# Kernel optimization log

Measured on AMD Instinct MI355X. Metric: run time of the kernel, lower is better.

Reference implementation:

```python
import jax, jax.numpy as jnp
import numpy as np

B, S, D, H, M = 2, 2048, 1024, 16, 40
DH = D // H  # 64
L = S + M    # kv length after memory concat


def setup_inputs() -> dict:
    key = jax.random.key(0)
    ks = jax.random.split(key, 20)
    s = 1.0 / np.sqrt(D)
    inp = {
        'v': jax.random.normal(ks[0], (B, S, D), jnp.float32),
        'k': jax.random.normal(ks[1], (B, S, D), jnp.float32),
        'q': jax.random.normal(ks[2], (B, S, D), jnp.float32),
        # additive binary mask (1 = masked out), broadcast over heads
        'mask': jax.random.randint(ks[3], (B, 1, S, L), 0, 2).astype(jnp.float32),
        'Wq': jax.random.normal(ks[4], (D, D), jnp.float32) * s,
        'bq': jnp.zeros((D,), jnp.float32),
        'Wk': jax.random.normal(ks[5], (D, D), jnp.float32) * s,
        'bk': jnp.zeros((D,), jnp.float32),
        'Wv': jax.random.normal(ks[6], (D, D), jnp.float32) * s,
        'bv': jnp.zeros((D,), jnp.float32),
        'k_memory': jax.random.normal(ks[7], (1, M, D), jnp.float32) * (1.0 / np.sqrt(DH)),
        'v_memory': jax.random.normal(ks[8], (1, M, D), jnp.float32) * (1.0 / np.sqrt(M)),
        'Wkm': jax.random.normal(ks[9], (D, D), jnp.float32) * s,
        'bkm': jnp.zeros((D,), jnp.float32),
        'Wvm': jax.random.normal(ks[10], (D, D), jnp.float32) * s,
        'bvm': jnp.zeros((D,), jnp.float32),
        'Wo': jax.random.normal(ks[11], (D, D), jnp.float32) * s,
        'bo': jnp.zeros((D,), jnp.float32),
    }
    return inp


def _split_heads(x):
    # [B, T, D] -> [B, H, T, DH]
    b, t, _ = x.shape
    return x.reshape(b, t, H, DH).transpose(0, 2, 1, 3)


def reference(v, k, q, mask, Wq, bq, Wk, bk, Wv, bv, k_memory, v_memory,
              Wkm, bkm, Wvm, bvm, Wo, bo):
    qp = q @ Wq + bq
    kp = k @ Wk + bk
    vp = v @ Wv + bv
    km = (k_memory @ Wkm + bkm)  # [1, M, D]
    vm = (v_memory @ Wvm + bvm)  # [1, M, D]
    kc = jnp.concatenate([kp, jnp.broadcast_to(km, (kp.shape[0], M, D))], axis=1)
    vc = jnp.concatenate([vp, jnp.broadcast_to(vm, (vp.shape[0], M, D))], axis=1)
    qh, kh, vh = _split_heads(qp), _split_heads(kc), _split_heads(vc)
    # scores: [B, H, S, L]
    scores = jnp.einsum('bhqd,bhkd->bhqk', qh, kh) / np.sqrt(DH)
    scores = scores + mask * (-1e9)
    attn = jax.nn.softmax(scores, axis=-1)
    ctx = jnp.einsum('bhqk,bhkd->bhqd', attn, vh)  # [B, H, S, DH]
    ctx = ctx.transpose(0, 2, 1, 3).reshape(ctx.shape[0], S, D)
    out = ctx @ Wo + bo
    return (out, attn)
```

## Files before the change

### kernel.cpp

```cpp
#include <hip/hip_runtime.h>
#include <hip/hip_bf16.h>

typedef __attribute__((ext_vector_type(8))) short short8v;
typedef __attribute__((ext_vector_type(4))) short short4v;
typedef __attribute__((ext_vector_type(4))) float f32x4;

constexpr int B_ = 2, S_ = 2048, H_ = 16, MM_ = 40;
constexpr int L_ = S_ + MM_;
constexpr int LP_ = 2112;
constexpr int NT_ = 33;
constexpr float QSCALE = 0.18033688011112042f;

struct S2 { short hi, lo; };
__device__ __forceinline__ S2 split2(float f) {
    unsigned u = __builtin_bit_cast(unsigned, f);
    short hi = (short)(u >> 16);
    float fh = __builtin_bit_cast(float, u & 0xFFFF0000u);
    float fl = f - fh;
    short lo = (short)(__builtin_bit_cast(unsigned, fl) >> 16);
    return {hi, lo};
}
__device__ __forceinline__ short f2bh(float f) {
    unsigned u = __builtin_bit_cast(unsigned, f);
    u = (u + 0x7FFFu + ((u >> 16) & 1u)) >> 16;
    return (short)u;
}
__device__ __forceinline__ f32x4 mfma16(short8v a, short8v b, f32x4 c) {
    return __builtin_amdgcn_mfma_f32_16x16x32_bf16(a, b, c, 0, 0, 0);
}
__device__ __forceinline__ unsigned cvt_pk_bf16(float a, float b) {
    unsigned r;
    asm("v_cvt_pk_bf16_f32 %0, %1, %2" : "=v"(r) : "v"(a), "v"(b));
    return r;
}

__global__ __launch_bounds__(256) void wsplit6_kernel(
    const float* __restrict__ W0, const float* __restrict__ W1,
    const float* __restrict__ W2, const float* __restrict__ W3,
    const float* __restrict__ W4, const float* __restrict__ W5,
    short* __restrict__ WT)
{
    const float* Ws[6] = {W0, W1, W2, W3, W4, W5};
    const float* W = Ws[blockIdx.z];
    short* WTh = WT + (size_t)blockIdx.z * 2097152;
    short* WTl = WTh + 1048576;
    __shared__ float T[64][68];
    const int t = threadIdx.x;
    const int k0 = blockIdx.x * 64, n0 = blockIdx.y * 64;
    {
        int r = t >> 2, c = (t & 3) * 16;
        const float* src = W + (size_t)(k0 + r) * 1024 + n0 + c;
        *(float4*)&T[r][c + 0]  = *(const float4*)(src + 0);
        *(float4*)&T[r][c + 4]  = *(const float4*)(src + 4);
        *(float4*)&T[r][c + 8]  = *(const float4*)(src + 8);
        *(float4*)&T[r][c + 12] = *(const float4*)(src + 12);
    }
    __syncthreads();
    {
        int n = t >> 2, ks = (t & 3) * 16;
        short8v h0, h1, l0, l1;
#pragma unroll
        for (int j = 0; j < 8; ++j) {
            S2 a = split2(T[ks + j][n]);     h0[j] = a.hi; l0[j] = a.lo;
            S2 b = split2(T[ks + 8 + j][n]); h1[j] = b.hi; l1[j] = b.lo;
        }
        size_t dst = (size_t)(n0 + n) * 1024 + k0 + ks;
        *(short8v*)(WTh + dst) = h0;  *(short8v*)(WTh + dst + 8) = h1;
        *(short8v*)(WTl + dst) = l0;  *(short8v*)(WTl + dst + 8) = l1;
    }
}

template<int ASRC>
__device__ __forceinline__ void gemm_core(
    const float* __restrict__ Af, const short* __restrict__ Ahg,
    const short* __restrict__ Alg, const short* __restrict__ WTh,
    const short* __restrict__ WTl, const float* __restrict__ bias,
    float bscale, float scale,
    short* __restrict__ Oh, short* __restrict__ Ol, float* __restrict__ Of,
    int M, int RPB, int TD, int loff, int omode, int bx, int by,
    int kbeg, int kend)
{
    __shared__ short Ah[128][40];
    __shared__ short Al[128][40];
    __shared__ short Bh[128][40];
    __shared__ short Bl[128][40];
    const int tid = threadIdx.x;
    const int lane = tid & 63, wid = tid >> 6;
    const int wr = wid >> 1, wc = wid & 1;
    const int row0 = by * 128, col0 = bx * 128;
    const int sr = tid >> 1, sc = (tid & 1) << 4;

    f32x4 acc[4][4] = {};

    for (int k0 = kbeg; k0 < kend; k0 += 32) {
        if (ASRC == 0) {
            float f[16];
            int gr = row0 + sr;
            if (gr < M) {
                const float* ap = Af + (size_t)gr * 1024 + k0 + sc;
                float4 a0 = *(const float4*)(ap + 0);
                float4 a1 = *(const float4*)(ap + 4);
                float4 a2 = *(const float4*)(ap + 8);
                float4 a3 = *(const float4*)(ap + 12);
                f[0]=a0.x; f[1]=a0.y; f[2]=a0.z; f[3]=a0.w;
                f[4]=a1.x; f[5]=a1.y; f[6]=a1.z; f[7]=a1.w;
                f[8]=a2.x; f[9]=a2.y; f[10]=a2.z; f[11]=a2.w;
                f[12]=a3.x; f[13]=a3.y; f[14]=a3.z; f[15]=a3.w;
            } else {
#pragma unroll
                for (int j = 0; j < 16; ++j) f[j] = 0.f;
            }
            short8v h0, h1, l0, l1;
#pragma unroll
            for (int j = 0; j < 8; ++j) {
                S2 s = split2(f[j]); h0[j] = s.hi; l0[j] = s.lo;
            }
#pragma unroll
            for (int j = 0; j < 8; ++j) {
                S2 s = split2(f[8 + j]); h1[j] = s.hi; l1[j] = s.lo;
            }
            *(short8v*)&Ah[sr][sc] = h0; *(short8v*)&Ah[sr][sc + 8] = h1;
            *(short8v*)&Al[sr][sc] = l0; *(short8v*)&Al[sr][sc + 8] = l1;
        } else {
            const short* ah = Ahg + (size_t)(row0 + sr) * 1024 + k0 + sc;
            const short* al = Alg + (size_t)(row0 + sr) * 1024 + k0 + sc;
            *(short8v*)&Ah[sr][sc]     = *(const short8v*)ah;
            *(short8v*)&Ah[sr][sc + 8] = *(const short8v*)(ah + 8);
            *(short8v*)&Al[sr][sc]     = *(const short8v*)al;
            *(short8v*)&Al[sr][sc + 8] = *(const short8v*)(al + 8);
        }
        {
            const short* bh = WTh + (size_t)(col0 + sr) * 1024 + k0 + sc;
            const short* bl = WTl + (size_t)(col0 + sr) * 1024 + k0 + sc;
            *(short8v*)&Bh[sr][sc]     = *(const short8v*)bh;
            *(short8v*)&Bh[sr][sc + 8] = *(const short8v*)(bh + 8);
            *(short8v*)&Bl[sr][sc]     = *(const short8v*)bl;
            *(short8v*)&Bl[sr][sc + 8] = *(const short8v*)(bl + 8);
        }
        __syncthreads();
        const int kof = (lane >> 4) << 3;
        const int ar = lane & 15;
        short8v afh[4], afl[4], bfh[4], bfl[4];
#pragma unroll
        for (int i = 0; i < 4; ++i) {
            afh[i] = *(const short8v*)&Ah[wr * 64 + i * 16 + ar][kof];
            afl[i] = *(const short8v*)&Al[wr * 64 + i * 16 + ar][kof];
            bfh[i] = *(const short8v*)&Bh[wc * 64 + i * 16 + ar][kof];
            bfl[i] = *(const short8v*)&Bl[wc * 64 + i * 16 + ar][kof];
        }
#pragma unroll
        for (int i = 0; i < 4; ++i)
#pragma unroll
            for (int j = 0; j < 4; ++j) {
                acc[i][j] = mfma16(afh[i], bfh[j], acc[i][j]);
                acc[i][j] = mfma16(afh[i], bfl[j], acc[i][j]);
                acc[i][j] = mfma16(afl[i], bfh[j], acc[i][j]);
            }
        __syncthreads();
    }

#pragma unroll
    for (int i = 0; i < 4; ++i) {
#pragma unroll
        for (int j = 0; j < 4; ++j) {
            int colb = col0 + wc * 64 + j * 16 + (lane & 15);
            float bv = bias[colb] * bscale;
            int rowb = row0 + wr * 64 + i * 16 + ((lane >> 4) << 2);
            if (omode == 2) {
                if (rowb < M) {
                    int bb = rowb / RPB, tt = rowb % RPB;
                    int hh = colb >> 6, dh = colb & 63;
                    short4v hs;
#pragma unroll
                    for (int r = 0; r < 4; ++r)
                        hs[r] = f2bh((acc[i][j][r] + bv) * scale);
                    size_t dst = ((size_t)(bb * H_ + hh) * 64 + dh) * LP_ + loff + tt;
                    *(short4v*)(Oh + dst) = hs;
                }
            } else {
#pragma unroll
                for (int r = 0; r < 4; ++r) {
                    int row = rowb + r;
                    if (row < M) {
                        float o = (acc[i][j][r] + bv) * scale;
                        int bb = row / RPB, tt = row % RPB;
                        if (omode == 0) {
                            Of[((size_t)bb * TD + loff + tt) * 1024 + colb] = o;
                        } else {
                            int hh = colb >> 6, dh = colb & 63;
                            size_t dst = ((size_t)(bb * H_ + hh) * TD + loff + tt) * 64 + dh;
                            S2 s = split2(o);
                            Oh[dst] = s.hi; Ol[dst] = s.lo;
                        }
                    }
                }
            }
        }
    }
}

__global__ __launch_bounds__(256) void qkv_gemm(
    const float* __restrict__ q_in, const float* __restrict__ k_in,
    const float* __restrict__ v_in, const float* __restrict__ kmem,
    const float* __restrict__ vmem, const short* __restrict__ WT,
    const float* __restrict__ bq, const float* __restrict__ bk,
    const float* __restrict__ bv, const float* __restrict__ bkm,
    const float* __restrict__ bvm,
    short* __restrict__ Qh, short* __restrict__ Ql,
    short* __restrict__ Kh, short* __restrict__ Kl, short* __restrict__ Vh,
    const float* __restrict__ mask, unsigned* __restrict__ mp)
{
    const int z = blockIdx.z;
    if (z == 3) {
        const int blk = blockIdx.y * 8 + blockIdx.x;
        for (int rr = 0; rr < 16; ++rr) {
            const int row = blk * 16 + rr;
            const float* mr = mask + (size_t)row * L_;
            unsigned* orow = mp + (size_t)row * 68;
            for (int wd = threadIdx.x; wd < 66; wd += 256) {
                int l0 = wd * 32;
                unsigned bits = 0u;
                int lim = (wd < 65) ? 32 : 8;
                for (int j = 0; j < lim; j += 4) {
                    float4 m4 = *(const float4*)(mr + l0 + j);
                    bits |= ((unsigned)(m4.x != 0.f)) << (j + 0);
                    bits |= ((unsigned)(m4.y != 0.f)) << (j + 1);
                    bits |= ((unsigned)(m4.z != 0.f)) << (j + 2);
                    bits |= ((unsigned)(m4.w != 0.f)) << (j + 3);
                }
                if (wd == 65) bits |= 0xFFFFFF00u;
                orow[wd] = bits;
            }
        }
        for (int k = threadIdx.x; k < 192; k += 256) {
            int g = blk * 192 + k;
            int rd = g / 24, l = L_ + g % 24;
            Vh[(size_t)rd * LP_ + l] = 0;
        }
        return;
    }
    if (z >= 4) {
        if (blockIdx.y != 0) return;
        const int which = (z - 4) >> 1, b = (z - 4) & 1;
        const float* A = which ? vmem : kmem;
        const short* WTh = WT + (size_t)(3 + which) * 2097152;
        const short* WTl = WTh + 1048576;
        const float* bias = which ? bvm : bkm;
        short* Oh = which ? (Vh + (size_t)b * H_ * 64 * LP_)
                          : (Kh + (size_t)b * H_ * LP_ * 64);
        short* Ol = which ? nullptr : (Kl + (size_t)b * H_ * LP_ * 64);
        gemm_core<0>(A, nullptr, nullptr, WTh, WTl, bias, 1.0f, 1.0f,
                     Oh, Ol, nullptr, 40, 40, LP_, S_, which ? 2 : 1,
                     blockIdx.x, 0, 0, 1024);
        return;
    }
    const float* A = (z == 0) ? q_in : (z == 1) ? k_in : v_in;
    const short* WTh = WT + (size_t)z * 2097152;
    const short* WTl = WTh + 1048576;
    const float* bias = (z == 0) ? bq : (z == 1) ? bk : bv;
    float scale = (z == 0) ? QSCALE : 1.0f;
    short* Oh = (z == 0) ? Qh : (z == 1) ? Kh : Vh;
    short* Ol = (z == 0) ? Ql : Kl;
    int omode = (z == 2) ? 2 : 1;
    int TD = (z == 0) ? S_ : LP_;
    gemm_core<0>(A, nullptr, nullptr, WTh, WTl, bias, 1.0f, scale,
                 Oh, Ol, nullptr, 4096, 2048, TD, 0, omode,
                 blockIdx.x, blockIdx.y, 0, 1024);
}

__global__ __launch_bounds__(256) void out_gemm(
    const short* __restrict__ Ch, const short* __restrict__ Cl,
    const short* __restrict__ WT, const float* __restrict__ bo,
    float* __restrict__ Po0, float* __restrict__ Po1)
{
    const int z = blockIdx.z;
    const short* WTh = WT + (size_t)5 * 2097152;
    gemm_core<1>(nullptr, Ch, Cl, WTh, WTh + 1048576, bo,
                 z == 0 ? 1.0f : 0.0f, 1.0f,
                 nullptr, nullptr, z == 0 ? Po0 : Po1, 4096, 2048, S_, 0, 0,
                 blockIdx.x, blockIdx.y, z * 512, z * 512 + 512);
}

__global__ __launch_bounds__(256) void attn4_kernel(
    const short* __restrict__ Qh, const short* __restrict__ Ql,
    const short* __restrict__ Kh, const short* __restrict__ Kl,
    const short* __restrict__ Vh, const unsigned* __restrict__ mp,
    float* __restrict__ attn, float* __restrict__ invg,
    short* __restrict__ Ch, short* __restrict__ Cl)
{
    __shared__ short KhB[2][64][64];
    __shared__ short KlB[2][64][64];
    __shared__ short VB[64][64];
    __shared__ short Ph[4][16][68];

    const int id = blockIdx.x;
    const int wg = (id & 7) * 64 + (id >> 3);
    const int bh = wg >> 4, qb2 = wg & 15;
    const int b = bh >> 4, h = bh & 15;
    const int lane = threadIdx.x & 63, w = threadIdx.x >> 6;
    const int lq = lane & 15, hi = lane >> 4;
    const int sw = lq & 7;
    const int q0A = qb2 * 128 + w * 16;
    const int q0B = q0A + 64;

    const char* kh_g = (const char*)(Kh + (size_t)bh * LP_ * 64);
    const char* kl_g = (const char*)(Kl + (size_t)bh * LP_ * 64);
    const char* v_g  = (const char*)(Vh + (size_t)bh * 64 * LP_);

    auto stage_k = [&](int buf, int tt) {
#pragma unroll
        for (int i = 0; i < 2; ++i) {
            int o = w * 2048 + i * 1024 + lane * 16;
            int r = o >> 7, c = (o >> 4) & 7;
            int cs = c ^ (r & 7);
            const char* sh = kh_g + (size_t)tt * 8192 + r * 128 + cs * 16;
            const char* sl = kl_g + (size_t)tt * 8192 + r * 128 + cs * 16;
            __builtin_amdgcn_global_load_lds((const void*)sh,
                (void*)((char*)&KhB[buf][0][0] + w * 2048 + i * 1024), 16, 0, 0);
            __builtin_amdgcn_global_load_lds((const void*)sl,
                (void*)((char*)&KlB[buf][0][0] + w * 2048 + i * 1024), 16, 0, 0);
        }
    };
    auto stage_v = [&](int tt) {
#pragma unroll
        for (int i = 0; i < 2; ++i) {
            int o = w * 2048 + i * 1024 + lane * 16;
            int dh = o >> 7, c = (o >> 4) & 7;
            int cs = c ^ (dh & 7);
            const char* src = v_g + (size_t)dh * (LP_ * 2) + (size_t)tt * 128 + cs * 16;
            __builtin_amdgcn_global_load_lds((const void*)src,
                (void*)((char*)&VB[0][0] + w * 2048 + i * 1024), 16, 0, 0);
        }
    };

    const size_t qbA = ((size_t)bh * S_ + q0A + lq) * 64 + hi * 8;
    const size_t qbB = ((size_t)bh * S_ + q0B + lq) * 64 + hi * 8;
    const short8v qh0A = *(const short8v*)(Qh + qbA);
    const short8v qh1A = *(const short8v*)(Qh + qbA + 32);
    const short8v ql0A = *(const short8v*)(Ql + qbA);
    const short8v ql1A = *(const short8v*)(Ql + qbA + 32);
    const short8v qh0B = *(const short8v*)(Qh + qbB);
    const short8v qh1B = *(const short8v*)(Qh + qbB + 32);
    const short8v ql0B = *(const short8v*)(Ql + qbB);
    const short8v ql1B = *(const short8v*)(Ql + qbB + 32);
    const unsigned* mrowA = mp + ((size_t)b * S_ + q0A + lq) * 68;
    const unsigned* mrowB = mp + ((size_t)b * S_ + q0B + lq) * 68;

    const int dr = lane >> 2, dc = lane & 3;
    short* dbaseA = (short*)(attn + ((size_t)bh * S_ + q0A - (w * 16) + (w * 16) + dr) * L_);
    dbaseA = (short*)(attn + ((size_t)bh * S_ + q0A + dr) * L_);
    short* dbaseB = (short*)(attn + ((size_t)bh * S_ + q0B + dr) * L_);

    float smA = 0.f, smB = 0.f;
    f32x4 pvA[4] = {};
    f32x4 pvB[4] = {};

    stage_k(0, 0);
    stage_v(0);
    __syncthreads();

    int cur = 0;
    for (int t = 0; t < NT_; ++t) {
        if (t < NT_ - 1) stage_k(cur ^ 1, t + 1);

        const short8v* kp = (const short8v*)&KhB[cur][0][0];
        const short8v* lp = (const short8v*)&KlB[cur][0][0];
        short8v kh0s[4], kh1s[4], kl0s[4], kl1s[4];
#pragma unroll
        for (int ls = 0; ls < 4; ++ls) {
            const int r = ls * 16 + lq;
            kh0s[ls] = kp[r * 8 + (hi ^ sw)];
            kh1s[ls] = kp[r * 8 + ((hi + 4) ^ sw)];
            kl0s[ls] = lp[r * 8 + (hi ^ sw)];
            kl1s[ls] = lp[r * 8 + ((hi + 4) ^ sw)];
        }
        const unsigned w0A = mrowA[2 * t], w1A = mrowA[2 * t + 1];
#pragma unroll
        for (int ls = 0; ls < 4; ++ls) {
            __builtin_amdgcn_s_setprio(1);
            f32x4 acc = {0.f, 0.f, 0.f, 0.f};
            acc = mfma16(kh0s[ls], qh0A, acc); acc = mfma16(kh1s[ls], qh1A, acc);
            acc = mfma16(kh0s[ls], ql0A, acc); acc = mfma16(kh1s[ls], ql1A, acc);
            acc = mfma16(kl0s[ls], qh0A, acc); acc = mfma16(kl1s[ls], qh1A, acc);
            __builtin_amdgcn_s_setprio(0);
            const unsigned wb = (ls & 2) ? w1A : w0A;
            const int sh = (ls & 1) * 16 + hi * 4;
            float pr[4];
#pragma unroll
            for (int r2 = 0; r2 < 4; ++r2) {
                float e = __builtin_exp2f(acc[r2]);
                pr[r2] = ((wb >> (sh + r2)) & 1u) ? 0.f : e;
            }
            smA += (pr[0] + pr[1]) + (pr[2] + pr[3]);
            *(uint2*)&Ph[w][lq][ls * 16 + hi * 4] =
                uint2{cvt_pk_bf16(pr[0], pr[1]), cvt_pk_bf16(pr[2], pr[3])};
        }
        {
            short8v v0 = *(const short8v*)&Ph[w][dr][dc * 8];
            short8v v1 = *(const short8v*)&Ph[w][dr][32 + dc * 8];
            short* dst = dbaseA + t * 64 + dc * 8;
            if (t < NT_ - 1) { *(short8v*)dst = v0; *(short8v*)(dst + 32) = v1; }
            else { *(short8v*)dst = v0; if (dc == 0) *(short8v*)(dst + 32) = v1; }
        }
        __syncthreads();
        {
            const short8v pa0 = *(const short8v*)&Ph[w][lq][hi * 8];
            const short8v pa1 = *(const short8v*)&Ph[w][lq][32 + hi * 8];
            const short8v* vp = (const short8v*)&VB[0][0];
            __builtin_amdgcn_s_setprio(1);
#pragma unroll
            for (int j = 0; j < 4; ++j)
                pvA[j] = mfma16(pa0, vp[(j * 16 + lq) * 8 + (hi ^ sw)], pvA[j]);
#pragma unroll
            for (int j = 0; j < 4; ++j)
                pvA[j] = mfma16(pa1, vp[(j * 16 + lq) * 8 + ((hi + 4) ^ sw)], pvA[j]);
            __builtin_amdgcn_s_setprio(0);
        }
        const unsigned w0B = mrowB[2 * t], w1B = mrowB[2 * t + 1];
#pragma unroll
        for (int ls = 0; ls < 4; ++ls) {
            __builtin_amdgcn_s_setprio(1);
            f32x4 acc = {0.f, 0.f, 0.f, 0.f};
            acc = mfma16(kh0s[ls], qh0B, acc); acc = mfma16(kh1s[ls], qh1B, acc);
            acc = mfma16(kh0s[ls], ql0B, acc); acc = mfma16(kh1s[ls], ql1B, acc);
            acc = mfma16(kl0s[ls], qh0B, acc); acc = mfma16(kl1s[ls], qh1B, acc);
            __builtin_amdgcn_s_setprio(0);
            const unsigned wb = (ls & 2) ? w1B : w0B;
            const int sh = (ls & 1) * 16 + hi * 4;
            float pr[4];
#pragma unroll
            for (int r2 = 0; r2 < 4; ++r2) {
                float e = __builtin_exp2f(acc[r2]);
                pr[r2] = ((wb >> (sh + r2)) & 1u) ? 0.f : e;
            }
            smB += (pr[0] + pr[1]) + (pr[2] + pr[3]);
            *(uint2*)&Ph[w][lq][ls * 16 + hi * 4] =
                uint2{cvt_pk_bf16(pr[0], pr[1]), cvt_pk_bf16(pr[2], pr[3])};
        }
        {
            short8v v0 = *(const short8v*)&Ph[w][dr][dc * 8];
            short8v v1 = *(const short8v*)&Ph[w][dr][32 + dc * 8];
            short* dst = dbaseB + t * 64 + dc * 8;
            if (t < NT_ - 1) { *(short8v*)dst = v0; *(short8v*)(dst + 32) = v1; }
            else { *(short8v*)dst = v0; if (dc == 0) *(short8v*)(dst + 32) = v1; }
        }
        {
            const short8v pa0 = *(const short8v*)&Ph[w][lq][hi * 8];
            const short8v pa1 = *(const short8v*)&Ph[w][lq][32 + hi * 8];
            const short8v* vp = (const short8v*)&VB[0][0];
            __builtin_amdgcn_s_setprio(1);
#pragma unroll
            for (int j = 0; j < 4; ++j)
                pvB[j] = mfma16(pa0, vp[(j * 16 + lq) * 8 + (hi ^ sw)], pvB[j]);
#pragma unroll
            for (int j = 0; j < 4; ++j)
                pvB[j] = mfma16(pa1, vp[(j * 16 + lq) * 8 + ((hi + 4) ^ sw)], pvB[j]);
            __builtin_amdgcn_s_setprio(0);
        }
        __syncthreads();
        if (t < NT_ - 1) stage_v(t + 1);
        cur ^= 1;
    }

    smA += __shfl_xor(smA, 16); smA += __shfl_xor(smA, 32);
    smB += __shfl_xor(smB, 16); smB += __shfl_xor(smB, 32);
    if (lane < 16) {
        invg[(size_t)bh * S_ + q0A + lane] = smA > 0.f ? 1.0f / smA : 0.f;
        invg[(size_t)bh * S_ + q0B + lane] = smB > 0.f ? 1.0f / smB : 0.f;
    }
#pragma unroll
    for (int r = 0; r < 4; ++r) {
        float svA = __shfl(smA, hi * 4 + r);
        float svB = __shfl(smB, hi * 4 + r);
        float ivA = svA > 0.f ? 1.0f / svA : 0.f;
        float ivB = svB > 0.f ? 1.0f / svB : 0.f;
#pragma unroll
        for (int j = 0; j < 4; ++j) {
            size_t dA = ((size_t)b * S_ + q0A + hi * 4 + r) * 1024 + h * 64 + j * 16 + lq;
            S2 sA = split2(pvA[j][r] * ivA);
            Ch[dA] = sA.hi; Cl[dA] = sA.lo;
            size_t dB = ((size_t)b * S_ + q0B + hi * 4 + r) * 1024 + h * 64 + j * 16 + lq;
            S2 sB = split2(pvB[j][r] * ivB);
            Ch[dB] = sB.hi; Cl[dB] = sB.lo;
        }
    }
}

__global__ __launch_bounds__(256) void norm_add(
    float* __restrict__ attn, const float* __restrict__ invg,
    const float* __restrict__ Po0, const float* __restrict__ Po1,
    float* __restrict__ outp)
{
    __shared__ unsigned rowbuf[1044];
    if (blockIdx.x >= 65536) {
        int i = ((blockIdx.x - 65536) * 256 + threadIdx.x) * 4;
        float4 a = *(const float4*)(Po0 + i);
        float4 bq = *(const float4*)(Po1 + i);
        a.x += bq.x; a.y += bq.y; a.z += bq.z; a.w += bq.w;
        *(float4*)(outp + i) = a;
        return;
    }
    const int row = blockIdx.x;
    const float iv = invg[row];
    float* rowp = attn + (size_t)row * L_;
    const unsigned* src = (const unsigned*)rowp;
    for (int i = threadIdx.x; i < 1044; i += 256) rowbuf[i] = src[i];
    __syncthreads();
    float4* dst = (float4*)rowp;
    for (int j = threadIdx.x; j < 522; j += 256) {
        unsigned u0 = rowbuf[2 * j], u1 = rowbuf[2 * j + 1];
        float4 v;
        v.x = __builtin_bit_cast(float, u0 << 16) * iv;
        v.y = __builtin_bit_cast(float, u0 & 0xFFFF0000u) * iv;
        v.z = __builtin_bit_cast(float, u1 << 16) * iv;
        v.w = __builtin_bit_cast(float, u1 & 0xFFFF0000u) * iv;
        dst[j] = v;
    }
}

extern "C" void kernel_launch(void* const* d_in, const int* in_sizes, int n_in,
                              void* d_out, int out_size, void* d_ws, size_t ws_size,
                              hipStream_t stream)
{
    const float* v_in = (const float*)d_in[0];
    const float* k_in = (const float*)d_in[1];
    const float* q_in = (const float*)d_in[2];
    const float* mask = (const float*)d_in[3];
    const float* Wq = (const float*)d_in[4];  const float* bq = (const float*)d_in[5];
    const float* Wk = (const float*)d_in[6];  const float* bk = (const float*)d_in[7];
    const float* Wv = (const float*)d_in[8];  const float* bv = (const float*)d_in[9];
    const float* kmem = (const float*)d_in[10];
    const float* vmem = (const float*)d_in[11];
    const float* Wkm = (const float*)d_in[12]; const float* bkm = (const float*)d_in[13];
    const float* Wvm = (const float*)d_in[14]; const float* bvm = (const float*)d_in[15];
    const float* Wo = (const float*)d_in[16];  const float* bo = (const float*)d_in[17];

    char* wsb = (char*)d_ws;
    short* WT  = (short*)(wsb);
    short* Qhb = (short*)(wsb + 25165824);
    short* Qlb = (short*)(wsb + 33554432);
    short* Khb = (short*)(wsb + 41943040);
    short* Klb = (short*)(wsb + 50593792);
    short* Vhb = (short*)(wsb + 59244544);
    short* Chb = (short*)(wsb + 67895296);
    short* Clb = (short*)(wsb + 76283904);
    float* invb = (float*)(wsb + 84672512);
    unsigned* mp = (unsigned*)(wsb + 84934656);
    if (ws_size < 86048768) return;
    float* Po0 = (float*)(wsb + 25165824);
    float* Po1 = (float*)(wsb + 41943040);

    float* outp = (float*)d_out;
    float* attnp = outp + (size_t)B_ * S_ * 1024;

    dim3 blk(256);

    wsplit6_kernel<<<dim3(16, 16, 6), blk, 0, stream>>>(Wq, Wk, Wv, Wkm, Wvm, Wo, WT);

    qkv_gemm<<<dim3(8, 32, 8), blk, 0, stream>>>(
        q_in, k_in, v_in, kmem, vmem, WT, bq, bk, bv, bkm, bvm,
        Qhb, Qlb, Khb, Klb, Vhb, mask, mp);

    attn4_kernel<<<dim3(512), blk, 0, stream>>>(
        Qhb, Qlb, Khb, Klb, Vhb, mp, attnp, invb, Chb, Clb);

    out_gemm<<<dim3(8, 32, 2), blk, 0, stream>>>(Chb, Clb, WT, bo, Po0, Po1);

    norm_add<<<dim3(65536 + 4096), blk, 0, stream>>>(attnp, invb, Po0, Po1, outp);
}
```

Measured before the change: 595.5 us.

## Fuse attention-probability normalization into attention kernel epilogue

The separate norm_add pass, which reread each packed bf16 attention row and rewrote it as normalized fp32, is removed. The attention kernel now does this itself in an epilogue: after a vmcnt wait, each wave reloads its own rows, scales them by the inverse row sum and writes fp32 in place. The output partial-sum add becomes a small standalone kernel. The mask-packing work is also moved to z==0 in qkv_gemm so it is scheduled first. This saves a launch and the invg buffer, but the epilogue is serialized (unroll 1) inside a 512-block kernel and depends on its own global stores being visible to later loads.

```diff
diff --git a/kernel.cpp b/kernel.cpp
--- a/kernel.cpp
+++ b/kernel.cpp
@@ -211,7 +211,7 @@
     const float* __restrict__ mask, unsigned* __restrict__ mp)
 {
     const int z = blockIdx.z;
-    if (z == 3) {
+    if (z == 0) {
         const int blk = blockIdx.y * 8 + blockIdx.x;
         for (int rr = 0; rr < 16; ++rr) {
             const int row = blk * 16 + rr;
@@ -254,15 +254,16 @@
                      blockIdx.x, 0, 0, 1024);
         return;
     }
-    const float* A = (z == 0) ? q_in : (z == 1) ? k_in : v_in;
-    const short* WTh = WT + (size_t)z * 2097152;
+    const int g = z - 1;
+    const float* A = (g == 0) ? q_in : (g == 1) ? k_in : v_in;
+    const short* WTh = WT + (size_t)g * 2097152;
     const short* WTl = WTh + 1048576;
-    const float* bias = (z == 0) ? bq : (z == 1) ? bk : bv;
-    float scale = (z == 0) ? QSCALE : 1.0f;
-    short* Oh = (z == 0) ? Qh : (z == 1) ? Kh : Vh;
-    short* Ol = (z == 0) ? Ql : Kl;
-    int omode = (z == 2) ? 2 : 1;
-    int TD = (z == 0) ? S_ : LP_;
+    const float* bias = (g == 0) ? bq : (g == 1) ? bk : bv;
+    float scale = (g == 0) ? QSCALE : 1.0f;
+    short* Oh = (g == 0) ? Qh : (g == 1) ? Kh : Vh;
+    short* Ol = (g == 0) ? Ql : Kl;
+    int omode = (g == 2) ? 2 : 1;
+    int TD = (g == 0) ? S_ : LP_;
     gemm_core<0>(A, nullptr, nullptr, WTh, WTl, bias, 1.0f, scale,
                  Oh, Ol, nullptr, 4096, 2048, TD, 0, omode,
                  blockIdx.x, blockIdx.y, 0, 1024);
@@ -281,11 +282,22 @@
                  blockIdx.x, blockIdx.y, z * 512, z * 512 + 512);
 }
 
+__global__ __launch_bounds__(256) void add_out(
+    const float* __restrict__ Po0, const float* __restrict__ Po1,
+    float* __restrict__ outp)
+{
+    int i = (blockIdx.x * 256 + threadIdx.x) * 4;
+    float4 a = *(const float4*)(Po0 + i);
+    float4 b = *(const float4*)(Po1 + i);
+    a.x += b.x; a.y += b.y; a.z += b.z; a.w += b.w;
+    *(float4*)(outp + i) = a;
+}
+
 __global__ __launch_bounds__(256) void attn4_kernel(
     const short* __restrict__ Qh, const short* __restrict__ Ql,
     const short* __restrict__ Kh, const short* __restrict__ Kl,
     const short* __restrict__ Vh, const unsigned* __restrict__ mp,
-    float* __restrict__ attn, float* __restrict__ invg,
+    float* __restrict__ attn,
     short* __restrict__ Ch, short* __restrict__ Cl)
 {
     __shared__ short KhB[2][64][64];
@@ -347,8 +359,7 @@
     const unsigned* mrowB = mp + ((size_t)b * S_ + q0B + lq) * 68;
 
     const int dr = lane >> 2, dc = lane & 3;
-    short* dbaseA = (short*)(attn + ((size_t)bh * S_ + q0A - (w * 16) + (w * 16) + dr) * L_);
-    dbaseA = (short*)(attn + ((size_t)bh * S_ + q0A + dr) * L_);
+    short* dbaseA = (short*)(attn + ((size_t)bh * S_ + q0A + dr) * L_);
     short* dbaseB = (short*)(attn + ((size_t)bh * S_ + q0B + dr) * L_);
 
     float smA = 0.f, smB = 0.f;
@@ -464,10 +475,7 @@
 
     smA += __shfl_xor(smA, 16); smA += __shfl_xor(smA, 32);
     smB += __shfl_xor(smB, 16); smB += __shfl_xor(smB, 32);
-    if (lane < 16) {
-        invg[(size_t)bh * S_ + q0A + lane] = smA > 0.f ? 1.0f / smA : 0.f;
-        invg[(size_t)bh * S_ + q0B + lane] = smB > 0.f ? 1.0f / smB : 0.f;
-    }
+
 #pragma unroll
     for (int r = 0; r < 4; ++r) {
         float svA = __shfl(smA, hi * 4 + r);
@@ -484,37 +492,38 @@
             Ch[dB] = sB.hi; Cl[dB] = sB.lo;
         }
     }
-}
-
-__global__ __launch_bounds__(256) void norm_add(
-    float* __restrict__ attn, const float* __restrict__ invg,
-    const float* __restrict__ Po0, const float* __restrict__ Po1,
-    float* __restrict__ outp)
-{
-    __shared__ unsigned rowbuf[1044];
-    if (blockIdx.x >= 65536) {
-        int i = ((blockIdx.x - 65536) * 256 + threadIdx.x) * 4;
-        float4 a = *(const float4*)(Po0 + i);
-        float4 bq = *(const float4*)(Po1 + i);
-        a.x += bq.x; a.y += bq.y; a.z += bq.z; a.w += bq.w;
-        *(float4*)(outp + i) = a;
-        return;
-    }
-    const int row = blockIdx.x;
-    const float iv = invg[row];
-    float* rowp = attn + (size_t)row * L_;
-    const unsigned* src = (const unsigned*)rowp;
-    for (int i = threadIdx.x; i < 1044; i += 256) rowbuf[i] = src[i];
-    __syncthreads();
-    float4* dst = (float4*)rowp;
-    for (int j = threadIdx.x; j < 522; j += 256) {
-        unsigned u0 = rowbuf[2 * j], u1 = rowbuf[2 * j + 1];
-        float4 v;
-        v.x = __builtin_bit_cast(float, u0 << 16) * iv;
-        v.y = __builtin_bit_cast(float, u0 & 0xFFFF0000u) * iv;
-        v.z = __builtin_bit_cast(float, u1 << 16) * iv;
-        v.w = __builtin_bit_cast(float, u1 & 0xFFFF0000u) * iv;
-        dst[j] = v;
+
+    asm volatile("s_waitcnt vmcnt(0)");
+#pragma unroll 1
+    for (int s = 0; s < 2; ++s) {
+        const int q0 = s ? q0B : q0A;
+        const float smv = s ? smB : smA;
+#pragma unroll 1
+        for (int i = 0; i < 16; ++i) {
+            float sv = __shfl(smv, i);
+            float iv = sv > 0.f ? 1.0f / sv : 0.f;
+            float* rowf = attn + ((size_t)bh * S_ + q0 + i) * L_;
+            unsigned* rw = (unsigned*)rowf;
+            unsigned u[17];
+#pragma unroll
+            for (int it = 0; it < 16; ++it) u[it] = rw[lane + it * 64];
+            if (lane < 20) u[16] = rw[lane + 1024];
+#pragma unroll
+            for (int it = 0; it < 16; ++it) {
+                unsigned uu = u[it];
+                float2 v;
+                v.x = __builtin_bit_cast(float, uu << 16) * iv;
+                v.y = __builtin_bit_cast(float, uu & 0xFFFF0000u) * iv;
+                *(float2*)(rowf + 2 * (lane + it * 64)) = v;
+            }
+            if (lane < 20) {
+                unsigned uu = u[16];
+                float2 v;
+                v.x = __builtin_bit_cast(float, uu << 16) * iv;
+                v.y = __builtin_bit_cast(float, uu & 0xFFFF0000u) * iv;
+                *(float2*)(rowf + 2 * (lane + 1024)) = v;
+            }
+        }
     }
 }
 
@@ -544,7 +553,6 @@
     short* Vhb = (short*)(wsb + 59244544);
     short* Chb = (short*)(wsb + 67895296);
     short* Clb = (short*)(wsb + 76283904);
-    float* invb = (float*)(wsb + 84672512);
     unsigned* mp = (unsigned*)(wsb + 84934656);
     if (ws_size < 86048768) return;
     float* Po0 = (float*)(wsb + 25165824);
@@ -562,9 +570,8 @@
         Qhb, Qlb, Khb, Klb, Vhb, mask, mp);
 
     attn4_kernel<<<dim3(512), blk, 0, stream>>>(
-        Qhb, Qlb, Khb, Klb, Vhb, mp, attnp, invb, Chb, Clb);
+        Qhb, Qlb, Khb, Klb, Vhb, mp, attnp, Chb, Clb);
 
     out_gemm<<<dim3(8, 32, 2), blk, 0, stream>>>(Chb, Clb, WT, bo, Po0, Po1);
-
-    norm_add<<<dim3(65536 + 4096), blk, 0, stream>>>(attnp, invb, Po0, Po1, outp);
-}
+    add_out<<<dim3(4096), blk, 0, stream>>>(Po0, Po1, outp);
+}
```

Result: faster. 571.6 us (-4.0%).
